# Optimization experiments

Measured on AMD Instinct MI355X. Metric: run time of the kernel, lower is better.

Reference implementation:

```python
import jax, jax.numpy as jnp
import numpy as np

N_NODES = 65536
NUM_GRAPHS = 128
NODES_PER_GRAPH = N_NODES // NUM_GRAPHS
HIDDEN = 512
EPS = 1e-6


def setup_inputs() -> dict:
    key = jax.random.key(0)
    k1, = jax.random.split(key, 1)
    x = jax.random.normal(k1, (N_NODES, HIDDEN), dtype=jnp.float32)
    gnw = jnp.ones((HIDDEN,), dtype=jnp.float32)
    gnb = jnp.zeros((HIDDEN,), dtype=jnp.float32)
    msc = jnp.ones((HIDDEN,), dtype=jnp.float32)
    batch_num = jnp.full((NUM_GRAPHS,), NODES_PER_GRAPH, dtype=jnp.int64)
    return {"x": x, "gnw": gnw, "gnb": gnb, "msc": msc, "batch_num": batch_num}


def reference(x, gnw, gnb, msc, batch_num):
    # x: [N, D] node features; batch_num: [B] per-graph node counts (sum == N)
    B = batch_num.shape[0]
    N = x.shape[0]
    seg = jnp.repeat(jnp.arange(B), batch_num, total_repeat_length=N)  # [N] graph id per node
    counts = batch_num.astype(x.dtype)[:, None]  # [B, 1]
    # per-graph mean: scatter-add then divide by segment size
    mean = jax.ops.segment_sum(x, seg, num_segments=B) / counts  # [B, D]
    sub = x - mean[seg] * msc  # [N, D]
    # per-graph variance of `sub` (matches original: second scatter_add of sub^2)
    var = jax.ops.segment_sum(sub * sub, seg, num_segments=B) / counts  # [B, D]
    std = jnp.sqrt(var + EPS)  # [B, D]
    return gnw * sub / std[seg] + gnb
```

## Files before the change

kernel.cpp:

```cpp
#include <hip/hip_runtime.h>


constexpr int N_NODES    = 65536;
constexpr int NUM_GRAPHS = 128;
constexpr int NPG        = N_NODES / NUM_GRAPHS;
constexpr int D          = 512;
constexpr int D4         = D / 4;
constexpr int SLICES     = 8;
constexpr int NS         = NPG / SLICES;
constexpr float EPS      = 1e-6f;

__global__ __launch_bounds__(128) void k_stats(const float* __restrict__ x,
                                               float* __restrict__ psum,
                                               float* __restrict__ psq) {
    const int g = blockIdx.x / SLICES;
    const int s = blockIdx.x % SLICES;
    const int t = threadIdx.x;

    const float4* xp = reinterpret_cast<const float4*>(x)
                     + (size_t)(g * NPG + s * NS) * D4 + t;

    float4 sum = make_float4(0.f, 0.f, 0.f, 0.f);
    float4 sq  = make_float4(0.f, 0.f, 0.f, 0.f);
    #pragma unroll 8
    for (int i = 0; i < NS; ++i) {
        float4 v = xp[(size_t)i * D4];
        sum.x += v.x; sum.y += v.y; sum.z += v.z; sum.w += v.w;
        sq.x = fmaf(v.x, v.x, sq.x);
        sq.y = fmaf(v.y, v.y, sq.y);
        sq.z = fmaf(v.z, v.z, sq.z);
        sq.w = fmaf(v.w, v.w, sq.w);
    }

    const size_t o = (size_t)(s * NUM_GRAPHS + g) * D4 + t;
    reinterpret_cast<float4*>(psum)[o] = sum;
    reinterpret_cast<float4*>(psq)[o]  = sq;
}

__global__ __launch_bounds__(256) void k_finalize(const float* __restrict__ psum,
                                                  const float* __restrict__ psq,
                                                  const float* __restrict__ gnw,
                                                  const float* __restrict__ gnb,
                                                  const float* __restrict__ msc,
                                                  float* __restrict__ Aarr,
                                                  float* __restrict__ Barr) {
    const int idx = blockIdx.x * 256 + threadIdx.x;
    const int g = idx / D;
    const int d = idx - g * D;

    float S1 = 0.f, S2 = 0.f;
    #pragma unroll
    for (int s = 0; s < SLICES; ++s) {
        const size_t o = (size_t)(s * NUM_GRAPHS + g) * D + d;
        S1 += psum[o];
        S2 += psq[o];
    }

    const float inv_n = 1.0f / (float)NPG;
    const float m   = S1 * inv_n;
    const float c   = m * msc[d];
    float var = S2 * inv_n - 2.0f * c * m + c * c;
    var = fmaxf(var, 0.0f);
    const float rstd = rsqrtf(var + EPS);
    const float A = gnw[d] * rstd;
    Aarr[idx] = A;
    Barr[idx] = fmaf(-A, c, gnb[d]);
}

constexpr int K2_ITERS = 16;

__global__ __launch_bounds__(256) void k_norm(const float* __restrict__ x,
                                              const float* __restrict__ Aarr,
                                              const float* __restrict__ Barr,
                                              float* __restrict__ out) {
    const int g  = blockIdx.x >> 4;
    const int d4 = threadIdx.x & (D4 - 1);

    const float4 a = reinterpret_cast<const float4*>(Aarr)[(size_t)g * D4 + d4];
    const float4 b = reinterpret_cast<const float4*>(Barr)[(size_t)g * D4 + d4];

    const float4* x4 = reinterpret_cast<const float4*>(x);
    float4*       o4 = reinterpret_cast<float4*>(out);

    const size_t i0 = (size_t)blockIdx.x * (256 * K2_ITERS) + threadIdx.x;
    #pragma unroll
    for (int it = 0; it < K2_ITERS; ++it) {
        const size_t i = i0 + (size_t)it * 256;
        float4 v = x4[i];
        float4 r;
        r.x = fmaf(a.x, v.x, b.x);
        r.y = fmaf(a.y, v.y, b.y);
        r.z = fmaf(a.z, v.z, b.z);
        r.w = fmaf(a.w, v.w, b.w);
        o4[i] = r;
    }
}

extern "C" void kernel_launch(void* const* d_in, const int* in_sizes, int n_in,
                              void* d_out, int out_size, void* d_ws, size_t ws_size,
                              hipStream_t stream) {
    const float* x   = (const float*)d_in[0];
    const float* gnw = (const float*)d_in[1];
    const float* gnb = (const float*)d_in[2];
    const float* msc = (const float*)d_in[3];
    float* out = (float*)d_out;

    float* ws   = (float*)d_ws;
    float* psum = ws;
    float* psq  = psum + (size_t)SLICES * NUM_GRAPHS * D;
    float* Aarr = psq  + (size_t)SLICES * NUM_GRAPHS * D;
    float* Barr = Aarr + (size_t)NUM_GRAPHS * D;

    k_stats<<<NUM_GRAPHS * SLICES, 128, 0, stream>>>(x, psum, psq);
    k_finalize<<<(NUM_GRAPHS * D) / 256, 256, 0, stream>>>(psum, psq, gnw, gnb,
                                                           msc, Aarr, Barr);
    const int n4 = (N_NODES * D) / 4;
    k_norm<<<n4 / (256 * K2_ITERS), 256, 0, stream>>>(x, Aarr, Barr, out);
}
```

Before: 259.1 us.

## Fuse stats, finalize and normalize into one per-graph kernel

Replaces the three-kernel pipeline with a single kernel where one 1024-thread block handles a whole graph. It computes sums in registers, reduces through shared memory, derives scale and shift, then re-reads the graph to write the output. This removes the workspace round trips and two launches, and relies on cache to serve the second read. The cost is launching only 128 blocks, which leaves many CUs idle on a device with more compute units.

```diff
diff --git a/kernel.cpp b/kernel.cpp
--- a/kernel.cpp
+++ b/kernel.cpp
@@ -6,93 +6,89 @@
 constexpr int NPG        = N_NODES / NUM_GRAPHS;
 constexpr int D          = 512;
 constexpr int D4         = D / 4;
-constexpr int SLICES     = 8;
-constexpr int NS         = NPG / SLICES;
+constexpr int RG         = 8;
+constexpr int ROWS_PER_T = NPG / RG;
 constexpr float EPS      = 1e-6f;
 
-__global__ __launch_bounds__(128) void k_stats(const float* __restrict__ x,
-                                               float* __restrict__ psum,
-                                               float* __restrict__ psq) {
-    const int g = blockIdx.x / SLICES;
-    const int s = blockIdx.x % SLICES;
-    const int t = threadIdx.x;
+__global__ __launch_bounds__(1024) void k_graphnorm(const float* __restrict__ x,
+                                                    const float* __restrict__ gnw,
+                                                    const float* __restrict__ gnb,
+                                                    const float* __restrict__ msc,
+                                                    float* __restrict__ out) {
+    __shared__ float4 lsum[RG][D4];
+    __shared__ float4 lsq [RG][D4];
+    __shared__ float4 lA[D4], lB[D4];
 
-    const float4* xp = reinterpret_cast<const float4*>(x)
-                     + (size_t)(g * NPG + s * NS) * D4 + t;
+    const int g   = blockIdx.x;
+    const int tid = threadIdx.x;
+    const int cq  = tid & (D4 - 1);
+    const int rg  = tid >> 7;
 
-    float4 sum = make_float4(0.f, 0.f, 0.f, 0.f);
-    float4 sq  = make_float4(0.f, 0.f, 0.f, 0.f);
+    const float4* xg = reinterpret_cast<const float4*>(x) + (size_t)g * NPG * D4;
+    float4*       og = reinterpret_cast<float4*>(out)     + (size_t)g * NPG * D4;
+
+    float4 s = make_float4(0.f, 0.f, 0.f, 0.f);
+    float4 q = make_float4(0.f, 0.f, 0.f, 0.f);
     #pragma unroll 8
-    for (int i = 0; i < NS; ++i) {
-        float4 v = xp[(size_t)i * D4];
-        sum.x += v.x; sum.y += v.y; sum.z += v.z; sum.w += v.w;
-        sq.x = fmaf(v.x, v.x, sq.x);
-        sq.y = fmaf(v.y, v.y, sq.y);
-        sq.z = fmaf(v.z, v.z, sq.z);
-        sq.w = fmaf(v.w, v.w, sq.w);
+    for (int i = 0; i < ROWS_PER_T; ++i) {
+        const int r = rg + i * RG;
+        float4 v = xg[(size_t)r * D4 + cq];
+        s.x += v.x; s.y += v.y; s.z += v.z; s.w += v.w;
+        q.x = fmaf(v.x, v.x, q.x);
+        q.y = fmaf(v.y, v.y, q.y);
+        q.z = fmaf(v.z, v.z, q.z);
+        q.w = fmaf(v.w, v.w, q.w);
     }
+    lsum[rg][cq] = s;
+    lsq [rg][cq] = q;
+    __syncthreads();
 
-    const size_t o = (size_t)(s * NUM_GRAPHS + g) * D4 + t;
-    reinterpret_cast<float4*>(psum)[o] = sum;
-    reinterpret_cast<float4*>(psq)[o]  = sq;
-}
+    if (tid < D4) {
+        const int d = tid;
+        float4 S1 = lsum[0][d], S2 = lsq[0][d];
+        #pragma unroll
+        for (int j = 1; j < RG; ++j) {
+            float4 a = lsum[j][d], b = lsq[j][d];
+            S1.x += a.x; S1.y += a.y; S1.z += a.z; S1.w += a.w;
+            S2.x += b.x; S2.y += b.y; S2.z += b.z; S2.w += b.w;
+        }
+        const float inv_n = 1.0f / (float)NPG;
+        const float4 w4 = reinterpret_cast<const float4*>(gnw)[d];
+        const float4 b4 = reinterpret_cast<const float4*>(gnb)[d];
+        const float4 m4 = reinterpret_cast<const float4*>(msc)[d];
+        float4 A, B;
+        {
+            float m, c, var, rstd;
+            m = S1.x * inv_n; c = m * m4.x;
+            var = fmaxf(fmaf(c, c, fmaf(-2.f * c, m, S2.x * inv_n)), 0.f);
+            rstd = rsqrtf(var + EPS); A.x = w4.x * rstd; B.x = fmaf(-A.x, c, b4.x);
+            m = S1.y * inv_n; c = m * m4.y;
+            var = fmaxf(fmaf(c, c, fmaf(-2.f * c, m, S2.y * inv_n)), 0.f);
+            rstd = rsqrtf(var + EPS); A.y = w4.y * rstd; B.y = fmaf(-A.y, c, b4.y);
+            m = S1.z * inv_n; c = m * m4.z;
+            var = fmaxf(fmaf(c, c, fmaf(-2.f * c, m, S2.z * inv_n)), 0.f);
+            rstd = rsqrtf(var + EPS); A.z = w4.z * rstd; B.z = fmaf(-A.z, c, b4.z);
+            m = S1.w * inv_n; c = m * m4.w;
+            var = fmaxf(fmaf(c, c, fmaf(-2.f * c, m, S2.w * inv_n)), 0.f);
+            rstd = rsqrtf(var + EPS); A.w = w4.w * rstd; B.w = fmaf(-A.w, c, b4.w);
+        }
+        lA[d] = A;
+        lB[d] = B;
+    }
+    __syncthreads();
 
-__global__ __launch_bounds__(256) void k_finalize(const float* __restrict__ psum,
-                                                  const float* __restrict__ psq,
-                                                  const float* __restrict__ gnw,
-                                                  const float* __restrict__ gnb,
-                                                  const float* __restrict__ msc,
-                                                  float* __restrict__ Aarr,
-                                                  float* __restrict__ Barr) {
-    const int idx = blockIdx.x * 256 + threadIdx.x;
-    const int g = idx / D;
-    const int d = idx - g * D;
-
-    float S1 = 0.f, S2 = 0.f;
-    #pragma unroll
-    for (int s = 0; s < SLICES; ++s) {
-        const size_t o = (size_t)(s * NUM_GRAPHS + g) * D + d;
-        S1 += psum[o];
-        S2 += psq[o];
-    }
-
-    const float inv_n = 1.0f / (float)NPG;
-    const float m   = S1 * inv_n;
-    const float c   = m * msc[d];
-    float var = S2 * inv_n - 2.0f * c * m + c * c;
-    var = fmaxf(var, 0.0f);
-    const float rstd = rsqrtf(var + EPS);
-    const float A = gnw[d] * rstd;
-    Aarr[idx] = A;
-    Barr[idx] = fmaf(-A, c, gnb[d]);
-}
-
-constexpr int K2_ITERS = 16;
-
-__global__ __launch_bounds__(256) void k_norm(const float* __restrict__ x,
-                                              const float* __restrict__ Aarr,
-                                              const float* __restrict__ Barr,
-                                              float* __restrict__ out) {
-    const int g  = blockIdx.x >> 4;
-    const int d4 = threadIdx.x & (D4 - 1);
-
-    const float4 a = reinterpret_cast<const float4*>(Aarr)[(size_t)g * D4 + d4];
-    const float4 b = reinterpret_cast<const float4*>(Barr)[(size_t)g * D4 + d4];
-
-    const float4* x4 = reinterpret_cast<const float4*>(x);
-    float4*       o4 = reinterpret_cast<float4*>(out);
-
-    const size_t i0 = (size_t)blockIdx.x * (256 * K2_ITERS) + threadIdx.x;
-    #pragma unroll
-    for (int it = 0; it < K2_ITERS; ++it) {
-        const size_t i = i0 + (size_t)it * 256;
-        float4 v = x4[i];
+    const float4 a = lA[cq];
+    const float4 b = lB[cq];
+    #pragma unroll 8
+    for (int i = 0; i < ROWS_PER_T; ++i) {
+        const size_t o = (size_t)(rg + i * RG) * D4 + cq;
+        float4 v = xg[o];
         float4 r;
         r.x = fmaf(a.x, v.x, b.x);
         r.y = fmaf(a.y, v.y, b.y);
         r.z = fmaf(a.z, v.z, b.z);
         r.w = fmaf(a.w, v.w, b.w);
-        o4[i] = r;
+        og[o] = r;
     }
 }
 
@@ -105,15 +101,5 @@
     const float* msc = (const float*)d_in[3];
     float* out = (float*)d_out;
 
-    float* ws   = (float*)d_ws;
-    float* psum = ws;
-    float* psq  = psum + (size_t)SLICES * NUM_GRAPHS * D;
-    float* Aarr = psq  + (size_t)SLICES * NUM_GRAPHS * D;
-    float* Barr = Aarr + (size_t)NUM_GRAPHS * D;
-
-    k_stats<<<NUM_GRAPHS * SLICES, 128, 0, stream>>>(x, psum, psq);
-    k_finalize<<<(NUM_GRAPHS * D) / 256, 256, 0, stream>>>(psum, psq, gnw, gnb,
-                                                           msc, Aarr, Barr);
-    const int n4 = (N_NODES * D) / 4;
-    k_norm<<<n4 / (256 * K2_ITERS), 256, 0, stream>>>(x, Aarr, Barr, out);
+    k_graphnorm<<<NUM_GRAPHS, 1024, 0, stream>>>(x, gnw, gnb, msc, out);
 }
```

New measurement: 253.1 us. 1.02x faster.
